# Kernel optimization log

Hardware: AMD Instinct MI355X
Metric: run time of the kernel (lower is better)

Reference implementation:

```python
import jax, jax.numpy as jnp
import numpy as np

B, H, L, D = 4, 16, 2048, 64
NEG = -1e9  # large negative for masked positions


def setup_inputs() -> dict:
    key = jax.random.key(0)
    kq, kk, kv, km, kb = jax.random.split(key, 5)
    Q = jax.random.normal(kq, (B, H, L, D), dtype=jnp.float32)
    K = jax.random.normal(kk, (B, H, L, D), dtype=jnp.float32)
    V = jax.random.normal(kv, (B, H, L, D), dtype=jnp.float32)
    attention_mask = jax.random.randint(km, (B, L), 0, 2, dtype=jnp.int32)
    attention_bias = jax.random.normal(kb, (B, L, L), dtype=jnp.float32)
    return {"Q": Q, "K": K, "V": V, "attention_mask": attention_mask,
            "attention_bias": attention_bias}


def reference(Q, K, V, attention_mask, attention_bias):
    scale = Q.shape[-1] ** 0.5
    # (b,h,l,l) = Q @ K^T / sqrt(d)
    score = jnp.einsum("bhqd,bhkd->bhqk", Q, K) / jnp.float32(scale)
    # bias (b,l,l) broadcasts over heads
    score = score + attention_bias[:, None, :, :]
    # mask (b,l): 1 valid, 0 invalid -> mask out key positions
    valid = attention_mask[:, None, None, :].astype(jnp.bool_)
    score = jnp.where(valid, score, jnp.float32(NEG))
    weight = jax.nn.softmax(score, axis=-1)
    # dropout p=0.0 -> identity
    return jnp.einsum("bhqk,bhkd->bhqd", weight, V)
```

## Files before the change

kernel.cpp:

```cpp
#include <hip/hip_runtime.h>


constexpr int kH = 16;
constexpr int kL = 2048;
constexpr int kD = 64;

typedef __attribute__((ext_vector_type(8))) short bf16x8;
typedef __attribute__((ext_vector_type(4))) float f32x4;

constexpr float kQScale = 0.125f * 1.44269504088896340736f;
constexpr float kL2E    = 1.44269504088896340736f;
constexpr float kNegBig = -1e9f;

__device__ __forceinline__ unsigned short f2bf(float f) {
  unsigned u = __float_as_uint(f);
  u += 0x7FFF + ((u >> 16) & 1);
  return (unsigned short)(u >> 16);
}
__device__ __forceinline__ unsigned pack2(float a, float b) {
  return (unsigned)f2bf(a) | ((unsigned)f2bf(b) << 16);
}
__device__ __forceinline__ unsigned cvt_pk_bf16(float lo, float hi) {
  unsigned r;
  asm("v_cvt_pk_bf16_f32 %0, %1, %2" : "=v"(r) : "v"(lo), "v"(hi));
  return r;
}
__device__ __forceinline__ float exp2_hw(float x) {
  float r; asm("v_exp_f32 %0, %1" : "=v"(r) : "v"(x)); return r;
}

__global__ __launch_bounds__(256, 4)
void attn_fwd(const float* __restrict__ Qg, const float* __restrict__ Kg,
              const float* __restrict__ Vg, const int* __restrict__ maskg,
              const float* __restrict__ biasg, float* __restrict__ outg) {
  __shared__ __align__(16) char smem[29696];
  unsigned short* const KsBase = (unsigned short*)smem;
  unsigned short* const VtBase = (unsigned short*)(smem + 9216);
  unsigned short* const QsAll  = (unsigned short*)smem;

  const int tid  = threadIdx.x;
  const int lane = tid & 63;
  const int w    = tid >> 6;
  const int col  = lane & 15;
  const int quad = lane >> 4;

  const int wg = blockIdx.x + (blockIdx.y << 4) + (blockIdx.z << 8);
  const int sw = ((wg & 7) << 7) | (wg >> 3);
  const int h  = sw & 15;
  const int qb = (sw >> 4) & 15;
  const int b  = sw >> 8;
  const int q0 = qb * 128;

  unsigned short* const Ps = (unsigned short*)(smem + 19456) + w * 1280;

  const size_t bh = (size_t)b * kH + h;
  const float4* const Q4 = (const float4*)(Qg + (bh * kL + q0) * kD);
  const float4* const K4 = (const float4*)(Kg + bh * kL * kD);
  const float4* const V4 = (const float4*)(Vg + bh * kL * kD);
  const float*  const brow = biasg + (size_t)b * kL * kL;
  const int*    const mrow = maskg + b * kL;

#pragma unroll
  for (int i = 0; i < 8; ++i) {
    const int slot = tid + i * 256;
    const int row = slot >> 4, dc = slot & 15;
    const float4 v = Q4[slot];
    *(uint2*)&QsAll[row * 72 + dc * 4] =
        make_uint2(cvt_pk_bf16(v.x * kQScale, v.y * kQScale),
                   cvt_pk_bf16(v.z * kQScale, v.w * kQScale));
  }
  __syncthreads();
  bf16x8 qf[2][2];
#pragma unroll
  for (int qt = 0; qt < 2; ++qt)
#pragma unroll
    for (int kc = 0; kc < 2; ++kc)
      qf[qt][kc] = *(const bf16x8*)
          &QsAll[(w * 32 + qt * 16 + col) * 72 + kc * 32 + quad * 8];
  __syncthreads();

  const int keyA = tid >> 4, dcA = tid & 15;
  const int jp   = tid >> 4, dcv = tid & 15;

  {
    const float4 a  = K4[keyA * 16 + dcA];
    const float4 c  = K4[(16 + keyA) * 16 + dcA];
    const float4 v0 = V4[(2 * jp) * 16 + dcv];
    const float4 v1 = V4[(2 * jp + 1) * 16 + dcv];
    *(uint2*)&KsBase[keyA * 72 + dcA * 4] =
        make_uint2(cvt_pk_bf16(a.x, a.y), cvt_pk_bf16(a.z, a.w));
    *(uint2*)&KsBase[(keyA + 16) * 72 + dcA * 4] =
        make_uint2(cvt_pk_bf16(c.x, c.y), cvt_pk_bf16(c.z, c.w));
    *(unsigned*)&VtBase[(dcv * 4 + 0) * 40 + 2 * jp] = pack2(v0.x, v1.x);
    *(unsigned*)&VtBase[(dcv * 4 + 1) * 40 + 2 * jp] = pack2(v0.y, v1.y);
    *(unsigned*)&VtBase[(dcv * 4 + 2) * 40 + 2 * jp] = pack2(v0.z, v1.z);
    *(unsigned*)&VtBase[(dcv * 4 + 3) * 40 + 2 * jp] = pack2(v0.w, v1.w);
  }

  f32x4 oacc[2][5];
  const f32x4 z4 = {0.f, 0.f, 0.f, 0.f};
#pragma unroll
  for (int qt = 0; qt < 2; ++qt)
#pragma unroll
    for (int dt = 0; dt < 5; ++dt) oacc[qt][dt] = z4;

  bf16x8 vones;
#pragma unroll
  for (int i = 0; i < 8; ++i) vones[i] = (short)0x3F80;

  const float* const bb =
      brow + (size_t)(q0 + w * 32 + quad * 4) * kL + col;

  for (int t = 0; t < 64; ++t) {
    const int buf = t & 1;
    const int k0 = t * 32;
    unsigned short* const Ks = KsBase + buf * 2304;
    unsigned short* const Vt = VtBase + buf * 2560;

    float4 pk0, pk1, pv0, pv1;
    const bool pf = (t < 63);
    if (pf) {
      const int kn = k0 + 32;
      pk0 = K4[(kn + keyA) * 16 + dcA];
      pk1 = K4[(kn + 16 + keyA) * 16 + dcA];
      pv0 = V4[(kn + 2 * jp) * 16 + dcv];
      pv1 = V4[(kn + 2 * jp + 1) * 16 + dcv];
    }

    const int mk0 = mrow[k0 + col];
    const int mk1 = mrow[k0 + 16 + col];
    const float sel0 = mk0 ? kL2E : 0.f, add0 = mk0 ? 0.f : kNegBig;
    const float sel1 = mk1 ? kL2E : 0.f, add1 = mk1 ? 0.f : kNegBig;
    float bt[2][4][2];
#pragma unroll
    for (int qt = 0; qt < 2; ++qt)
#pragma unroll
      for (int r = 0; r < 4; ++r) {
        const float* bp = bb + (size_t)(qt * 16 + r) * kL + k0;
        bt[qt][r][0] = fmaf(bp[0], sel0, add0);
        bt[qt][r][1] = fmaf(bp[16], sel1, add1);
      }

    __syncthreads();

    f32x4 sacc[2][2];
#pragma unroll
    for (int qt = 0; qt < 2; ++qt) { sacc[qt][0] = z4; sacc[qt][1] = z4; }
#pragma unroll
    for (int kc = 0; kc < 2; ++kc) {
      const bf16x8 bk0 = *(const bf16x8*)&Ks[col * 72 + kc * 32 + quad * 8];
      const bf16x8 bk1 = *(const bf16x8*)&Ks[(16 + col) * 72 + kc * 32 + quad * 8];
#pragma unroll
      for (int qt = 0; qt < 2; ++qt) {
        sacc[qt][0] = __builtin_amdgcn_mfma_f32_16x16x32_bf16(
            qf[qt][kc], bk0, sacc[qt][0], 0, 0, 0);
        sacc[qt][1] = __builtin_amdgcn_mfma_f32_16x16x32_bf16(
            qf[qt][kc], bk1, sacc[qt][1], 0, 0, 0);
      }
    }

#pragma unroll
    for (int qt = 0; qt < 2; ++qt)
#pragma unroll
      for (int r = 0; r < 4; ++r) {
        const float p0 = exp2_hw(sacc[qt][0][r] + bt[qt][r][0]);
        const float p1 = exp2_hw(sacc[qt][1][r] + bt[qt][r][1]);
        const int prow = (qt * 16 + quad * 4 + r) * 40;
        Ps[prow + col]      = (unsigned short)((__float_as_uint(p0) + 0x8000) >> 16);
        Ps[prow + 16 + col] = (unsigned short)((__float_as_uint(p1) + 0x8000) >> 16);
      }
    asm volatile("" ::: "memory");

    bf16x8 ap[2];
#pragma unroll
    for (int qt = 0; qt < 2; ++qt)
      ap[qt] = *(const bf16x8*)&Ps[(qt * 16 + col) * 40 + quad * 8];
#pragma unroll
    for (int dt = 0; dt < 4; ++dt) {
      const bf16x8 bv = *(const bf16x8*)&Vt[(dt * 16 + col) * 40 + quad * 8];
#pragma unroll
      for (int qt = 0; qt < 2; ++qt)
        oacc[qt][dt] = __builtin_amdgcn_mfma_f32_16x16x32_bf16(
            ap[qt], bv, oacc[qt][dt], 0, 0, 0);
    }
#pragma unroll
    for (int qt = 0; qt < 2; ++qt)
      oacc[qt][4] = __builtin_amdgcn_mfma_f32_16x16x32_bf16(
          ap[qt], vones, oacc[qt][4], 0, 0, 0);

    if (pf) {
      unsigned short* const Ksn = KsBase + (buf ^ 1) * 2304;
      unsigned short* const Vtn = VtBase + (buf ^ 1) * 2560;
      *(uint2*)&Ksn[keyA * 72 + dcA * 4] =
          make_uint2(cvt_pk_bf16(pk0.x, pk0.y), cvt_pk_bf16(pk0.z, pk0.w));
      *(uint2*)&Ksn[(keyA + 16) * 72 + dcA * 4] =
          make_uint2(cvt_pk_bf16(pk1.x, pk1.y), cvt_pk_bf16(pk1.z, pk1.w));
      *(unsigned*)&Vtn[(dcv * 4 + 0) * 40 + 2 * jp] = pack2(pv0.x, pv1.x);
      *(unsigned*)&Vtn[(dcv * 4 + 1) * 40 + 2 * jp] = pack2(pv0.y, pv1.y);
      *(unsigned*)&Vtn[(dcv * 4 + 2) * 40 + 2 * jp] = pack2(pv0.z, pv1.z);
      *(unsigned*)&Vtn[(dcv * 4 + 3) * 40 + 2 * jp] = pack2(pv0.w, pv1.w);
    }
  }

  float* const orow = outg + (bh * kL + q0) * kD;
#pragma unroll
  for (int qt = 0; qt < 2; ++qt)
#pragma unroll
    for (int r = 0; r < 4; ++r) {
      const float li = 1.0f / oacc[qt][4][r];
      float* op = orow + (size_t)(w * 32 + qt * 16 + quad * 4 + r) * kD + col;
#pragma unroll
      for (int dt = 0; dt < 4; ++dt)
        op[dt * 16] = oacc[qt][dt][r] * li;
    }
}

extern "C" void kernel_launch(void* const* d_in, const int* in_sizes, int n_in,
                              void* d_out, int out_size, void* d_ws, size_t ws_size,
                              hipStream_t stream) {
  const float* Q    = (const float*)d_in[0];
  const float* K    = (const float*)d_in[1];
  const float* V    = (const float*)d_in[2];
  const int*   mask = (const int*)d_in[3];
  const float* bias = (const float*)d_in[4];
  float* out = (float*)d_out;

  dim3 grid(kH, kL / 128, 4);
  dim3 block(256);
  attn_fwd<<<grid, block, 0, stream>>>(Q, K, V, mask, bias, out);
}
```

Baseline: 297.3 us.

## Double query tile per block to 256 rows with 512 threads and split K/V loaders

```diff
diff --git a/kernel.cpp b/kernel.cpp
--- a/kernel.cpp
+++ b/kernel.cpp
@@ -29,11 +29,11 @@
   float r; asm("v_exp_f32 %0, %1" : "=v"(r) : "v"(x)); return r;
 }
 
-__global__ __launch_bounds__(256, 4)
+__global__ __launch_bounds__(512, 4)
 void attn_fwd(const float* __restrict__ Qg, const float* __restrict__ Kg,
               const float* __restrict__ Vg, const int* __restrict__ maskg,
               const float* __restrict__ biasg, float* __restrict__ outg) {
-  __shared__ __align__(16) char smem[29696];
+  __shared__ __align__(16) char smem[39936];
   unsigned short* const KsBase = (unsigned short*)smem;
   unsigned short* const VtBase = (unsigned short*)(smem + 9216);
   unsigned short* const QsAll  = (unsigned short*)smem;
@@ -44,12 +44,12 @@
   const int col  = lane & 15;
   const int quad = lane >> 4;
 
-  const int wg = blockIdx.x + (blockIdx.y << 4) + (blockIdx.z << 8);
-  const int sw = ((wg & 7) << 7) | (wg >> 3);
+  const int wg = blockIdx.x + (blockIdx.y << 4) + (blockIdx.z << 7);
+  const int sw = ((wg & 7) << 6) | (wg >> 3);
   const int h  = sw & 15;
-  const int qb = (sw >> 4) & 15;
-  const int b  = sw >> 8;
-  const int q0 = qb * 128;
+  const int qb = (sw >> 4) & 7;
+  const int b  = sw >> 7;
+  const int q0 = qb * 256;
 
   unsigned short* const Ps = (unsigned short*)(smem + 19456) + w * 1280;
 
@@ -62,7 +62,7 @@
 
 #pragma unroll
   for (int i = 0; i < 8; ++i) {
-    const int slot = tid + i * 256;
+    const int slot = tid + i * 512;
     const int row = slot >> 4, dc = slot & 15;
     const float4 v = Q4[slot];
     *(uint2*)&QsAll[row * 72 + dc * 4] =
@@ -79,22 +79,25 @@
           &QsAll[(w * 32 + qt * 16 + col) * 72 + kc * 32 + quad * 8];
   __syncthreads();
 
-  const int keyA = tid >> 4, dcA = tid & 15;
-  const int jp   = tid >> 4, dcv = tid & 15;
-
-  {
-    const float4 a  = K4[keyA * 16 + dcA];
-    const float4 c  = K4[(16 + keyA) * 16 + dcA];
+  const int tidK = tid & 255;
+  const int keyA = tidK >> 4, dcA = tidK & 15;
+  const int jp   = tidK >> 4, dcv = tidK & 15;
+  const bool isV = (tid < 256);
+
+  if (isV) {
     const float4 v0 = V4[(2 * jp) * 16 + dcv];
     const float4 v1 = V4[(2 * jp + 1) * 16 + dcv];
+    *(unsigned*)&VtBase[(dcv * 4 + 0) * 40 + 2 * jp] = pack2(v0.x, v1.x);
+    *(unsigned*)&VtBase[(dcv * 4 + 1) * 40 + 2 * jp] = pack2(v0.y, v1.y);
+    *(unsigned*)&VtBase[(dcv * 4 + 2) * 40 + 2 * jp] = pack2(v0.z, v1.z);
+    *(unsigned*)&VtBase[(dcv * 4 + 3) * 40 + 2 * jp] = pack2(v0.w, v1.w);
+  } else {
+    const float4 a = K4[keyA * 16 + dcA];
+    const float4 c = K4[(16 + keyA) * 16 + dcA];
     *(uint2*)&KsBase[keyA * 72 + dcA * 4] =
         make_uint2(cvt_pk_bf16(a.x, a.y), cvt_pk_bf16(a.z, a.w));
     *(uint2*)&KsBase[(keyA + 16) * 72 + dcA * 4] =
         make_uint2(cvt_pk_bf16(c.x, c.y), cvt_pk_bf16(c.z, c.w));
-    *(unsigned*)&VtBase[(dcv * 4 + 0) * 40 + 2 * jp] = pack2(v0.x, v1.x);
-    *(unsigned*)&VtBase[(dcv * 4 + 1) * 40 + 2 * jp] = pack2(v0.y, v1.y);
-    *(unsigned*)&VtBase[(dcv * 4 + 2) * 40 + 2 * jp] = pack2(v0.z, v1.z);
-    *(unsigned*)&VtBase[(dcv * 4 + 3) * 40 + 2 * jp] = pack2(v0.w, v1.w);
   }
 
   f32x4 oacc[2][5];
@@ -117,14 +120,17 @@
     unsigned short* const Ks = KsBase + buf * 2304;
     unsigned short* const Vt = VtBase + buf * 2560;
 
-    float4 pk0, pk1, pv0, pv1;
+    float4 pa, pb;
     const bool pf = (t < 63);
     if (pf) {
       const int kn = k0 + 32;
-      pk0 = K4[(kn + keyA) * 16 + dcA];
-      pk1 = K4[(kn + 16 + keyA) * 16 + dcA];
-      pv0 = V4[(kn + 2 * jp) * 16 + dcv];
-      pv1 = V4[(kn + 2 * jp + 1) * 16 + dcv];
+      if (isV) {
+        pa = V4[(kn + 2 * jp) * 16 + dcv];
+        pb = V4[(kn + 2 * jp + 1) * 16 + dcv];
+      } else {
+        pa = K4[(kn + keyA) * 16 + dcA];
+        pb = K4[(kn + 16 + keyA) * 16 + dcA];
+      }
     }
 
     const int mk0 = mrow[k0 + col];
@@ -189,16 +195,19 @@
           ap[qt], vones, oacc[qt][4], 0, 0, 0);
 
     if (pf) {
-      unsigned short* const Ksn = KsBase + (buf ^ 1) * 2304;
-      unsigned short* const Vtn = VtBase + (buf ^ 1) * 2560;
-      *(uint2*)&Ksn[keyA * 72 + dcA * 4] =
-          make_uint2(cvt_pk_bf16(pk0.x, pk0.y), cvt_pk_bf16(pk0.z, pk0.w));
-      *(uint2*)&Ksn[(keyA + 16) * 72 + dcA * 4] =
-          make_uint2(cvt_pk_bf16(pk1.x, pk1.y), cvt_pk_bf16(pk1.z, pk1.w));
-      *(unsigned*)&Vtn[(dcv * 4 + 0) * 40 + 2 * jp] = pack2(pv0.x, pv1.x);
-      *(unsigned*)&Vtn[(dcv * 4 + 1) * 40 + 2 * jp] = pack2(pv0.y, pv1.y);
-      *(unsigned*)&Vtn[(dcv * 4 + 2) * 40 + 2 * jp] = pack2(pv0.z, pv1.z);
-      *(unsigned*)&Vtn[(dcv * 4 + 3) * 40 + 2 * jp] = pack2(pv0.w, pv1.w);
+      if (isV) {
+        unsigned short* const Vtn = VtBase + (buf ^ 1) * 2560;
+        *(unsigned*)&Vtn[(dcv * 4 + 0) * 40 + 2 * jp] = pack2(pa.x, pb.x);
+        *(unsigned*)&Vtn[(dcv * 4 + 1) * 40 + 2 * jp] = pack2(pa.y, pb.y);
+        *(unsigned*)&Vtn[(dcv * 4 + 2) * 40 + 2 * jp] = pack2(pa.z, pb.z);
+        *(unsigned*)&Vtn[(dcv * 4 + 3) * 40 + 2 * jp] = pack2(pa.w, pb.w);
+      } else {
+        unsigned short* const Ksn = KsBase + (buf ^ 1) * 2304;
+        *(uint2*)&Ksn[keyA * 72 + dcA * 4] =
+            make_uint2(cvt_pk_bf16(pa.x, pa.y), cvt_pk_bf16(pa.z, pa.w));
+        *(uint2*)&Ksn[(keyA + 16) * 72 + dcA * 4] =
+            make_uint2(cvt_pk_bf16(pb.x, pb.y), cvt_pk_bf16(pb.z, pb.w));
+      }
     }
   }
 
@@ -225,7 +234,7 @@
   const float* bias = (const float*)d_in[4];
   float* out = (float*)d_out;
 
-  dim3 grid(kH, kL / 128, 4);
-  dim3 block(256);
+  dim3 grid(kH, kL / 256, 4);
+  dim3 block(512);
   attn_fwd<<<grid, block, 0, stream>>>(Q, K, V, mask, bias, out);
 }
```

Result: slower. 310.8 us (+4.5%).
